# Performance work log

Hardware: AMD Instinct MI355X
Metric: run time of the kernel (lower is better)

The kernel has to match this reference:

```python
import jax, jax.numpy as jnp
import numpy as np

MARGIN_SCALE = 0.2
SPATIAL_ALPHA = 0.6
CHANNEL_ALPHA = 0.5
LANG_ALPHA = 0.4
EPS = 1e-06


def _xywh_to_xyxy(boxes):
    xc, yc, w, h = jnp.split(boxes, 4, axis=-1)
    return jnp.concatenate([xc - w / 2.0, yc - h / 2.0, xc + w / 2.0, yc + h / 2.0], axis=-1)


def _clamp_boxes(boxes):
    x1, y1, x2, y2 = [jnp.clip(b[..., 0], 0.0, 1.0) for b in jnp.split(boxes, 4, axis=-1)]
    x_low, x_high = jnp.minimum(x1, x2), jnp.maximum(x1, x2)
    y_low, y_high = jnp.minimum(y1, y2), jnp.maximum(y1, y2)
    w = jnp.maximum(x_high - x_low, EPS)
    h = jnp.maximum(y_high - y_low, EPS)
    cx = (x_high + x_low) * 0.5
    cy = (y_high + y_low) * 0.5
    return jnp.stack([
        jnp.clip(cx - w * 0.5, 0.0, 1.0),
        jnp.clip(cy - h * 0.5, 0.0, 1.0),
        jnp.clip(cx + w * 0.5, 0.0, 1.0),
        jnp.clip(cy + h * 0.5, 0.0, 1.0),
    ], axis=-1)


def _box_to_mask(boxes_xyxy, H, W, margin, dtype):
    # fully vectorized replacement of the per-sample Python loop
    ys = jnp.linspace(0.0, 1.0, H)  # [H]
    xs = jnp.linspace(0.0, 1.0, W)  # [W]
    x1, y1, x2, y2 = [boxes_xyxy[:, i] for i in range(4)]
    mx1 = jnp.clip(x1 - margin, 0.0, 1.0)[:, None, None]
    my1 = jnp.clip(y1 - margin, 0.0, 1.0)[:, None, None]
    mx2 = jnp.clip(x2 + margin, 0.0, 1.0)[:, None, None]
    my2 = jnp.clip(y2 + margin, 0.0, 1.0)[:, None, None]
    xg = xs[None, None, :]  # [1,1,W]
    yg = ys[None, :, None]  # [1,H,1]
    mask = (xg >= mx1) & (xg <= mx2) & (yg >= my1) & (yg <= my2)  # [B,H,W]
    return mask.astype(dtype)[:, None, :, :]  # [B,1,H,W]


def _conv2d(x, w, b, pad):
    out = jax.lax.conv_general_dilated(
        x, w, window_strides=(1, 1), padding=((pad, pad), (pad, pad)),
        dimension_numbers=('NCHW', 'OIHW', 'NCHW'))
    return out + b[None, :, None, None]


def setup_inputs() -> dict:
    key = jax.random.key(0)
    ks = jax.random.split(key, 9)
    B, C, H, W = 32, 256, 64, 64
    s = lambda fan_in: 1.0 / np.sqrt(fan_in)
    return {
        'feat': jax.random.normal(ks[0], (B, C, H, W), jnp.float32),
        'lang_vec': jax.random.normal(ks[1], (B, 256), jnp.float32),
        'pointer_xywh': jax.random.uniform(ks[2], (B, 4), jnp.float32),
        'conv1_w': jax.random.normal(ks[3], (16, 1, 3, 3), jnp.float32) * s(9),
        'conv1_b': jnp.zeros((16,), jnp.float32),
        'conv2_w': jax.random.normal(ks[4], (1, 16, 1, 1), jnp.float32) * s(16),
        'conv2_b': jnp.zeros((1,), jnp.float32),
        'cg_w1': jax.random.normal(ks[5], (256, 512), jnp.float32) * s(512),
        'cg_b1': jnp.zeros((256,), jnp.float32),
        'cg_w2': jax.random.normal(ks[6], (256, 256), jnp.float32) * s(256),
        'cg_b2': jnp.zeros((256,), jnp.float32),
        'lf_w1': jax.random.normal(ks[7], (256, 512), jnp.float32) * s(512),
        'lf_b1': jnp.zeros((256,), jnp.float32),
        'lf_w2': jax.random.normal(ks[8], (256, 256), jnp.float32) * s(256),
        'lf_b2': jnp.zeros((256,), jnp.float32),
    }


def reference(feat, lang_vec, pointer_xywh, conv1_w, conv1_b, conv2_w, conv2_b,
              cg_w1, cg_b1, cg_w2, cg_b2, lf_w1, lf_b1, lf_w2, lf_b2):
    B, C, H, W = feat.shape
    boxes_xyxy = _clamp_boxes(_xywh_to_xyxy(pointer_xywh))
    w = jnp.maximum(boxes_xyxy[:, 2] - boxes_xyxy[:, 0], 1e-4)
    h = jnp.maximum(boxes_xyxy[:, 3] - boxes_xyxy[:, 1], 1e-4)
    diag = jnp.sqrt(w * w + h * h)
    margin = jnp.clip(diag * MARGIN_SCALE, 0.02, 0.2)
    mask = _box_to_mask(boxes_xyxy, H, W, margin, feat.dtype)  # [B,1,H,W]

    # spatial gate: conv3x3 -> relu -> conv1x1 -> sigmoid
    hidden = jax.nn.relu(_conv2d(mask, conv1_w, conv1_b, pad=1))
    refined_mask = jax.nn.sigmoid(_conv2d(hidden, conv2_w, conv2_b, pad=0))  # [B,1,H,W]

    mask_area = jnp.maximum(refined_mask.sum(axis=(2, 3)), 1.0)  # [B,1]
    pointer_feat = (feat * refined_mask).sum(axis=(2, 3)) / mask_area  # [B,C]

    fusion = jnp.concatenate([pointer_feat, lang_vec], axis=1)  # [B, C+256]
    ch_gate = jax.nn.sigmoid(jax.nn.relu(fusion @ cg_w1.T + cg_b1) @ cg_w2.T + cg_b2)
    ch_gate = ch_gate.reshape(B, C, 1, 1)
    lang_delta = jnp.tanh(jax.nn.relu(fusion @ lf_w1.T + lf_b1) @ lf_w2.T + lf_b2)

    guided_feat = feat * (1.0 + SPATIAL_ALPHA * refined_mask) * (1.0 + CHANNEL_ALPHA * ch_gate)
    guided_lang = lang_vec + LANG_ALPHA * lang_delta
    return (guided_feat, guided_lang, boxes_xyxy, refined_mask, pointer_feat)
```

## Files before the change

kernel.cpp:

```cpp
#include <hip/hip_runtime.h>
#include <math.h>

#define B_  32
#define C_  256
#define H_  64
#define W_  64
#define HW  (H_*W_)
#define HW4 (HW/4)
#define RPB 4

typedef float f32x4 __attribute__((ext_vector_type(4)));

__device__ __forceinline__ float clamp01(float v) {
    return fminf(fmaxf(v, 0.0f), 1.0f);
}

__global__ __launch_bounds__(256) void kern_mask(
    const float* __restrict__ xywh,
    const float* __restrict__ conv1_w, const float* __restrict__ conv1_b,
    const float* __restrict__ conv2_w, const float* __restrict__ conv2_b,
    float* __restrict__ out_boxes, float* __restrict__ out_rm,
    float* __restrict__ ws_part)
{
    const int b = blockIdx.x >> 2;
    const int q = blockIdx.x & 3;
    const int t = threadIdx.x;

    __shared__ float sw1[16 * 9];
    __shared__ float sb1[16];
    __shared__ float sw2[16];
    __shared__ float sred[4];

    if (t < 144)                 sw1[t]       = conv1_w[t];
    else if (t < 160)            sb1[t - 144] = conv1_b[t - 144];
    else if (t < 176)            sw2[t - 160] = conv2_w[t - 160];
    const float b2v = conv2_b[0];

    const float xc = xywh[b * 4 + 0];
    const float yc = xywh[b * 4 + 1];
    const float bw = xywh[b * 4 + 2];
    const float bh = xywh[b * 4 + 3];

    float x1 = clamp01(xc - bw * 0.5f);
    float y1 = clamp01(yc - bh * 0.5f);
    float x2 = clamp01(xc + bw * 0.5f);
    float y2 = clamp01(yc + bh * 0.5f);
    float xl = fminf(x1, x2), xh = fmaxf(x1, x2);
    float yl = fminf(y1, y2), yh = fmaxf(y1, y2);
    float w_ = fmaxf(xh - xl, 1e-6f);
    float h_ = fmaxf(yh - yl, 1e-6f);
    float cx = (xh + xl) * 0.5f, cy = (yh + yl) * 0.5f;
    float bx1 = clamp01(cx - w_ * 0.5f);
    float by1 = clamp01(cy - h_ * 0.5f);
    float bx2 = clamp01(cx + w_ * 0.5f);
    float by2 = clamp01(cy + h_ * 0.5f);

    if (t == 0 && q == 0) {
        out_boxes[b * 4 + 0] = bx1;
        out_boxes[b * 4 + 1] = by1;
        out_boxes[b * 4 + 2] = bx2;
        out_boxes[b * 4 + 3] = by2;
    }

    float ww = fmaxf(bx2 - bx1, 1e-4f);
    float hh = fmaxf(by2 - by1, 1e-4f);
    float diag = sqrtf(ww * ww + hh * hh);
    float margin = fminf(fmaxf(diag * 0.2f, 0.02f), 0.2f);
    float mx1 = clamp01(bx1 - margin);
    float my1 = clamp01(by1 - margin);
    float mx2 = clamp01(bx2 + margin);
    float my2 = clamp01(by2 + margin);

    __syncthreads();

    float asum = 0.0f;
    const int p0 = q * 1024;
    for (int pi = t; pi < 1024; pi += 256) {
        const int p = p0 + pi;
        const int y = p >> 6;
        const int x = p & 63;
        float mv[9];
        #pragma unroll
        for (int ky = 0; ky < 3; ++ky) {
            const int yy = y + ky - 1;
            float gy = (float)((double)yy / 63.0);
            bool yin = (yy >= 0) && (yy < H_) && (gy >= my1) && (gy <= my2);
            #pragma unroll
            for (int kx = 0; kx < 3; ++kx) {
                const int xx = x + kx - 1;
                float gx = (float)((double)xx / 63.0);
                bool xin = (xx >= 0) && (xx < W_) && (gx >= mx1) && (gx <= mx2);
                mv[ky * 3 + kx] = (yin && xin) ? 1.0f : 0.0f;
            }
        }
        float z = b2v;
        #pragma unroll
        for (int oc = 0; oc < 16; ++oc) {
            float hsum = sb1[oc];
            #pragma unroll
            for (int k = 0; k < 9; ++k) hsum = fmaf(mv[k], sw1[oc * 9 + k], hsum);
            z = fmaf(fmaxf(hsum, 0.0f), sw2[oc], z);
        }
        float rm = 1.0f / (1.0f + expf(-z));
        out_rm[b * HW + p] = rm;
        asum += rm;
    }

    #pragma unroll
    for (int off = 32; off > 0; off >>= 1) asum += __shfl_down(asum, off, 64);
    int lane = t & 63, wid = t >> 6;
    if (lane == 0) sred[wid] = asum;
    __syncthreads();
    if (t == 0) ws_part[b * 4 + q] = sred[0] + sred[1] + sred[2] + sred[3];
}

__global__ __launch_bounds__(256) void kern_pf_fused(
    const float* __restrict__ feat, const float* __restrict__ rm,
    const float* __restrict__ ws_part, float* __restrict__ out_pf,
    float* __restrict__ out_gf)
{
    const int blk = blockIdx.x;
    const int b = blk >> 6;
    const int c0 = (blk & 63) * RPB;
    __shared__ f32x4 sred[4];

    const size_t row0 = ((size_t)b * C_ + c0) * HW;
    const f32x4* fr = (const f32x4*)(feat + row0);
    f32x4* orow = (f32x4*)(out_gf + row0);
    const f32x4* r4 = (const f32x4*)(rm + (size_t)b * HW);

    float s0 = 0.f, s1 = 0.f, s2 = 0.f, s3 = 0.f;
    for (int i = threadIdx.x; i < HW4; i += 256) {
        f32x4 r = r4[i];
        f32x4 m;
        m.x = 1.0f + 0.6f * r.x;
        m.y = 1.0f + 0.6f * r.y;
        m.z = 1.0f + 0.6f * r.z;
        m.w = 1.0f + 0.6f * r.w;

        f32x4 f0 = __builtin_nontemporal_load(&fr[i]);
        f32x4 f1 = __builtin_nontemporal_load(&fr[i + HW4]);
        f32x4 f2 = __builtin_nontemporal_load(&fr[i + 2 * HW4]);
        f32x4 f3 = __builtin_nontemporal_load(&fr[i + 3 * HW4]);

        s0 = fmaf(f0.x, r.x, fmaf(f0.y, r.y, fmaf(f0.z, r.z, fmaf(f0.w, r.w, s0))));
        s1 = fmaf(f1.x, r.x, fmaf(f1.y, r.y, fmaf(f1.z, r.z, fmaf(f1.w, r.w, s1))));
        s2 = fmaf(f2.x, r.x, fmaf(f2.y, r.y, fmaf(f2.z, r.z, fmaf(f2.w, r.w, s2))));
        s3 = fmaf(f3.x, r.x, fmaf(f3.y, r.y, fmaf(f3.z, r.z, fmaf(f3.w, r.w, s3))));

        f32x4 o0, o1, o2, o3;
        o0.x = f0.x * m.x; o0.y = f0.y * m.y; o0.z = f0.z * m.z; o0.w = f0.w * m.w;
        o1.x = f1.x * m.x; o1.y = f1.y * m.y; o1.z = f1.z * m.z; o1.w = f1.w * m.w;
        o2.x = f2.x * m.x; o2.y = f2.y * m.y; o2.z = f2.z * m.z; o2.w = f2.w * m.w;
        o3.x = f3.x * m.x; o3.y = f3.y * m.y; o3.z = f3.z * m.z; o3.w = f3.w * m.w;
        orow[i]           = o0;
        orow[i + HW4]     = o1;
        orow[i + 2*HW4]   = o2;
        orow[i + 3*HW4]   = o3;
    }

    #pragma unroll
    for (int off = 32; off > 0; off >>= 1) {
        s0 += __shfl_down(s0, off, 64);
        s1 += __shfl_down(s1, off, 64);
        s2 += __shfl_down(s2, off, 64);
        s3 += __shfl_down(s3, off, 64);
    }
    int lane = threadIdx.x & 63, wid = threadIdx.x >> 6;
    if (lane == 0) { f32x4 v; v.x = s0; v.y = s1; v.z = s2; v.w = s3; sred[wid] = v; }
    __syncthreads();
    if (threadIdx.x == 0) {
        float area = fmaxf(ws_part[b * 4 + 0] + ws_part[b * 4 + 1] +
                           ws_part[b * 4 + 2] + ws_part[b * 4 + 3], 1.0f);
        float inv = 1.0f / area;
        f32x4 t0 = sred[0], t1 = sred[1], t2 = sred[2], t3 = sred[3];
        out_pf[b * C_ + c0 + 0] = (t0.x + t1.x + t2.x + t3.x) * inv;
        out_pf[b * C_ + c0 + 1] = (t0.y + t1.y + t2.y + t3.y) * inv;
        out_pf[b * C_ + c0 + 2] = (t0.z + t1.z + t2.z + t3.z) * inv;
        out_pf[b * C_ + c0 + 3] = (t0.w + t1.w + t2.w + t3.w) * inv;
    }
}

__global__ __launch_bounds__(256) void kern_mlp(
    const float* __restrict__ pf, const float* __restrict__ lang,
    const float* __restrict__ cg_w1, const float* __restrict__ cg_b1,
    const float* __restrict__ cg_w2, const float* __restrict__ cg_b2,
    const float* __restrict__ lf_w1, const float* __restrict__ lf_b1,
    const float* __restrict__ lf_w2, const float* __restrict__ lf_b2,
    float* __restrict__ ws_cg, float* __restrict__ out_gl)
{
    const int b = blockIdx.x >> 1;
    const int which = blockIdx.x & 1;
    const int t = threadIdx.x;
    __shared__ float fus[512];
    __shared__ float hid[256];

    fus[t]       = pf[b * 256 + t];
    fus[256 + t] = lang[b * 256 + t];

    const float* w1 = which ? lf_w1 : cg_w1;
    const float* b1 = which ? lf_b1 : cg_b1;
    const float* w2 = which ? lf_w2 : cg_w2;
    const float* b2 = which ? lf_b2 : cg_b2;
    __syncthreads();

    const f32x4* wv = (const f32x4*)(w1 + (size_t)t * 512);
    const f32x4* fv = (const f32x4*)fus;
    float s = 0.0f;
    #pragma unroll 4
    for (int k = 0; k < 128; ++k) {
        f32x4 f = fv[k], w = wv[k];
        s = fmaf(f.x, w.x, fmaf(f.y, w.y, fmaf(f.z, w.z, fmaf(f.w, w.w, s))));
    }
    hid[t] = fmaxf(s + b1[t], 0.0f);
    __syncthreads();

    const f32x4* w2v = (const f32x4*)(w2 + (size_t)t * 256);
    const f32x4* hv = (const f32x4*)hid;
    float s2 = 0.0f;
    #pragma unroll 4
    for (int k = 0; k < 64; ++k) {
        f32x4 h = hv[k], w = w2v[k];
        s2 = fmaf(h.x, w.x, fmaf(h.y, w.y, fmaf(h.z, w.z, fmaf(h.w, w.w, s2))));
    }
    s2 += b2[t];
    if (which == 0) {
        ws_cg[b * 256 + t] = 1.0f / (1.0f + expf(-s2));
    } else {
        out_gl[b * 256 + t] = fus[256 + t] + 0.4f * tanhf(s2);
    }
}

__global__ __launch_bounds__(256) void kern_scale(
    const float* __restrict__ ws_cg, float* __restrict__ out_gf)
{
    const int blk = blockIdx.x;
    const int b = blk >> 6;
    const int c0 = (blk & 63) * RPB;
    const float g0 = 1.0f + 0.5f * ws_cg[b * C_ + c0 + 0];
    const float g1 = 1.0f + 0.5f * ws_cg[b * C_ + c0 + 1];
    const float g2 = 1.0f + 0.5f * ws_cg[b * C_ + c0 + 2];
    const float g3 = 1.0f + 0.5f * ws_cg[b * C_ + c0 + 3];

    f32x4* o = (f32x4*)(out_gf + ((size_t)b * C_ + c0) * HW);

    for (int i = threadIdx.x; i < HW4; i += 256) {
        f32x4 a = o[i];
        f32x4 b1v = o[i + HW4];
        f32x4 c = o[i + 2 * HW4];
        f32x4 d = o[i + 3 * HW4];
        a.x *= g0; a.y *= g0; a.z *= g0; a.w *= g0;
        b1v.x *= g1; b1v.y *= g1; b1v.z *= g1; b1v.w *= g1;
        c.x *= g2; c.y *= g2; c.z *= g2; c.w *= g2;
        d.x *= g3; d.y *= g3; d.z *= g3; d.w *= g3;
        o[i]           = a;
        o[i + HW4]     = b1v;
        o[i + 2*HW4]   = c;
        o[i + 3*HW4]   = d;
    }
}

extern "C" void kernel_launch(void* const* d_in, const int* in_sizes, int n_in,
                              void* d_out, int out_size, void* d_ws, size_t ws_size,
                              hipStream_t stream) {
    const float* feat     = (const float*)d_in[0];
    const float* lang     = (const float*)d_in[1];
    const float* xywh     = (const float*)d_in[2];
    const float* conv1_w  = (const float*)d_in[3];
    const float* conv1_b  = (const float*)d_in[4];
    const float* conv2_w  = (const float*)d_in[5];
    const float* conv2_b  = (const float*)d_in[6];
    const float* cg_w1    = (const float*)d_in[7];
    const float* cg_b1    = (const float*)d_in[8];
    const float* cg_w2    = (const float*)d_in[9];
    const float* cg_b2    = (const float*)d_in[10];
    const float* lf_w1    = (const float*)d_in[11];
    const float* lf_b1    = (const float*)d_in[12];
    const float* lf_w2    = (const float*)d_in[13];
    const float* lf_b2    = (const float*)d_in[14];

    float* out = (float*)d_out;
    const size_t N_GF = (size_t)B_ * C_ * HW;
    float* out_gf    = out;
    float* out_gl    = out_gf + N_GF;
    float* out_boxes = out_gl + (size_t)B_ * C_;
    float* out_rm    = out_boxes + B_ * 4;
    float* out_pf    = out_rm + (size_t)B_ * HW;

    float* wsf     = (float*)d_ws;
    float* ws_part = wsf;
    float* ws_cg   = wsf + 128;

    (void)ws_size; (void)in_sizes; (void)n_in; (void)out_size;

    kern_mask<<<B_ * 4, 256, 0, stream>>>(xywh, conv1_w, conv1_b, conv2_w, conv2_b,
                                          out_boxes, out_rm, ws_part);
    kern_pf_fused<<<B_ * C_ / RPB, 256, 0, stream>>>(feat, out_rm, ws_part,
                                                     out_pf, out_gf);
    kern_mlp<<<B_ * 2, 256, 0, stream>>>(out_pf, lang,
                                         cg_w1, cg_b1, cg_w2, cg_b2,
                                         lf_w1, lf_b1, lf_w2, lf_b2,
                                         ws_cg, out_gl);
    kern_scale<<<B_ * C_ / RPB, 256, 0, stream>>>(ws_cg, out_gf);
}
```

Measured before the change: 116.5 us.

## Split pooling from output write and fuse spatial and channel scaling in one pass

The first pass over the features now only computes the masked channel sums and no longer writes an intermediate guided output. A later kernel re-reads the features and applies both the spatial and channel gates in one write with nontemporal stores. This replaces a read-modify-write of the whole output with a second read of the input, cutting total DRAM traffic. The channel gate's affine form is also folded into the MLP kernel.

```diff
diff --git a/kernel.cpp b/kernel.cpp
--- a/kernel.cpp
+++ b/kernel.cpp
@@ -114,10 +114,9 @@
     if (t == 0) ws_part[b * 4 + q] = sred[0] + sred[1] + sred[2] + sred[3];
 }
 
-__global__ __launch_bounds__(256) void kern_pf_fused(
+__global__ __launch_bounds__(256) void kern_pf(
     const float* __restrict__ feat, const float* __restrict__ rm,
-    const float* __restrict__ ws_part, float* __restrict__ out_pf,
-    float* __restrict__ out_gf)
+    const float* __restrict__ ws_part, float* __restrict__ out_pf)
 {
     const int blk = blockIdx.x;
     const int b = blk >> 6;
@@ -126,37 +125,19 @@
 
     const size_t row0 = ((size_t)b * C_ + c0) * HW;
     const f32x4* fr = (const f32x4*)(feat + row0);
-    f32x4* orow = (f32x4*)(out_gf + row0);
     const f32x4* r4 = (const f32x4*)(rm + (size_t)b * HW);
 
     float s0 = 0.f, s1 = 0.f, s2 = 0.f, s3 = 0.f;
     for (int i = threadIdx.x; i < HW4; i += 256) {
         f32x4 r = r4[i];
-        f32x4 m;
-        m.x = 1.0f + 0.6f * r.x;
-        m.y = 1.0f + 0.6f * r.y;
-        m.z = 1.0f + 0.6f * r.z;
-        m.w = 1.0f + 0.6f * r.w;
-
-        f32x4 f0 = __builtin_nontemporal_load(&fr[i]);
-        f32x4 f1 = __builtin_nontemporal_load(&fr[i + HW4]);
-        f32x4 f2 = __builtin_nontemporal_load(&fr[i + 2 * HW4]);
-        f32x4 f3 = __builtin_nontemporal_load(&fr[i + 3 * HW4]);
-
+        f32x4 f0 = fr[i];
+        f32x4 f1 = fr[i + HW4];
+        f32x4 f2 = fr[i + 2 * HW4];
+        f32x4 f3 = fr[i + 3 * HW4];
         s0 = fmaf(f0.x, r.x, fmaf(f0.y, r.y, fmaf(f0.z, r.z, fmaf(f0.w, r.w, s0))));
         s1 = fmaf(f1.x, r.x, fmaf(f1.y, r.y, fmaf(f1.z, r.z, fmaf(f1.w, r.w, s1))));
         s2 = fmaf(f2.x, r.x, fmaf(f2.y, r.y, fmaf(f2.z, r.z, fmaf(f2.w, r.w, s2))));
         s3 = fmaf(f3.x, r.x, fmaf(f3.y, r.y, fmaf(f3.z, r.z, fmaf(f3.w, r.w, s3))));
-
-        f32x4 o0, o1, o2, o3;
-        o0.x = f0.x * m.x; o0.y = f0.y * m.y; o0.z = f0.z * m.z; o0.w = f0.w * m.w;
-        o1.x = f1.x * m.x; o1.y = f1.y * m.y; o1.z = f1.z * m.z; o1.w = f1.w * m.w;
-        o2.x = f2.x * m.x; o2.y = f2.y * m.y; o2.z = f2.z * m.z; o2.w = f2.w * m.w;
-        o3.x = f3.x * m.x; o3.y = f3.y * m.y; o3.z = f3.z * m.z; o3.w = f3.w * m.w;
-        orow[i]           = o0;
-        orow[i + HW4]     = o1;
-        orow[i + 2*HW4]   = o2;
-        orow[i + 3*HW4]   = o3;
     }
 
     #pragma unroll
@@ -225,38 +206,53 @@
     }
     s2 += b2[t];
     if (which == 0) {
-        ws_cg[b * 256 + t] = 1.0f / (1.0f + expf(-s2));
+        ws_cg[b * 256 + t] = 1.0f + 0.5f / (1.0f + expf(-s2));
     } else {
         out_gl[b * 256 + t] = fus[256 + t] + 0.4f * tanhf(s2);
     }
 }
 
-__global__ __launch_bounds__(256) void kern_scale(
+__global__ __launch_bounds__(256) void kern_guided(
+    const float* __restrict__ feat, const float* __restrict__ rm,
     const float* __restrict__ ws_cg, float* __restrict__ out_gf)
 {
     const int blk = blockIdx.x;
     const int b = blk >> 6;
     const int c0 = (blk & 63) * RPB;
-    const float g0 = 1.0f + 0.5f * ws_cg[b * C_ + c0 + 0];
-    const float g1 = 1.0f + 0.5f * ws_cg[b * C_ + c0 + 1];
-    const float g2 = 1.0f + 0.5f * ws_cg[b * C_ + c0 + 2];
-    const float g3 = 1.0f + 0.5f * ws_cg[b * C_ + c0 + 3];
-
-    f32x4* o = (f32x4*)(out_gf + ((size_t)b * C_ + c0) * HW);
+    const float g0 = ws_cg[b * C_ + c0 + 0];
+    const float g1 = ws_cg[b * C_ + c0 + 1];
+    const float g2 = ws_cg[b * C_ + c0 + 2];
+    const float g3 = ws_cg[b * C_ + c0 + 3];
+
+    const size_t row0 = ((size_t)b * C_ + c0) * HW;
+    const f32x4* fr = (const f32x4*)(feat + row0);
+    f32x4* orow = (f32x4*)(out_gf + row0);
+    const f32x4* r4 = (const f32x4*)(rm + (size_t)b * HW);
 
     for (int i = threadIdx.x; i < HW4; i += 256) {
-        f32x4 a = o[i];
-        f32x4 b1v = o[i + HW4];
-        f32x4 c = o[i + 2 * HW4];
-        f32x4 d = o[i + 3 * HW4];
-        a.x *= g0; a.y *= g0; a.z *= g0; a.w *= g0;
-        b1v.x *= g1; b1v.y *= g1; b1v.z *= g1; b1v.w *= g1;
-        c.x *= g2; c.y *= g2; c.z *= g2; c.w *= g2;
-        d.x *= g3; d.y *= g3; d.z *= g3; d.w *= g3;
-        o[i]           = a;
-        o[i + HW4]     = b1v;
-        o[i + 2*HW4]   = c;
-        o[i + 3*HW4]   = d;
+        f32x4 r = r4[i];
+        f32x4 m;
+        m.x = 1.0f + 0.6f * r.x;
+        m.y = 1.0f + 0.6f * r.y;
+        m.z = 1.0f + 0.6f * r.z;
+        m.w = 1.0f + 0.6f * r.w;
+        f32x4 f0 = fr[i];
+        f32x4 f1 = fr[i + HW4];
+        f32x4 f2 = fr[i + 2 * HW4];
+        f32x4 f3 = fr[i + 3 * HW4];
+        f32x4 o0, o1, o2, o3;
+        o0.x = f0.x * m.x * g0; o0.y = f0.y * m.y * g0;
+        o0.z = f0.z * m.z * g0; o0.w = f0.w * m.w * g0;
+        o1.x = f1.x * m.x * g1; o1.y = f1.y * m.y * g1;
+        o1.z = f1.z * m.z * g1; o1.w = f1.w * m.w * g1;
+        o2.x = f2.x * m.x * g2; o2.y = f2.y * m.y * g2;
+        o2.z = f2.z * m.z * g2; o2.w = f2.w * m.w * g2;
+        o3.x = f3.x * m.x * g3; o3.y = f3.y * m.y * g3;
+        o3.z = f3.z * m.z * g3; o3.w = f3.w * m.w * g3;
+        __builtin_nontemporal_store(o0, &orow[i]);
+        __builtin_nontemporal_store(o1, &orow[i + HW4]);
+        __builtin_nontemporal_store(o2, &orow[i + 2 * HW4]);
+        __builtin_nontemporal_store(o3, &orow[i + 3 * HW4]);
     }
 }
 
@@ -295,11 +291,10 @@
 
     kern_mask<<<B_ * 4, 256, 0, stream>>>(xywh, conv1_w, conv1_b, conv2_w, conv2_b,
                                           out_boxes, out_rm, ws_part);
-    kern_pf_fused<<<B_ * C_ / RPB, 256, 0, stream>>>(feat, out_rm, ws_part,
-                                                     out_pf, out_gf);
+    kern_pf<<<B_ * C_ / RPB, 256, 0, stream>>>(feat, out_rm, ws_part, out_pf);
     kern_mlp<<<B_ * 2, 256, 0, stream>>>(out_pf, lang,
                                          cg_w1, cg_b1, cg_w2, cg_b2,
                                          lf_w1, lf_b1, lf_w2, lf_b2,
                                          ws_cg, out_gl);
-    kern_scale<<<B_ * C_ / RPB, 256, 0, stream>>>(ws_cg, out_gf);
-}
+    kern_guided<<<B_ * C_ / RPB, 256, 0, stream>>>(feat, out_rm, ws_cg, out_gf);
+}
```

Result: faster. 95.00 us (-18.5%).
